# Kernel tuning notes

Hardware: AMD Instinct MI355X
Metric: run time of the kernel (lower is better)

Reference implementation:

```python
import jax, jax.numpy as jnp
import numpy as np

B, S, HID = 2, 2048, 2048
NH, NKV, D = 16, 8, 128
N_REP = NH // NKV
EPS = 1e-6
THETA = 10000.0


def setup_inputs() -> dict:
    key = jax.random.key(0)
    ks = jax.random.split(key, 6)
    s = 0.02
    return {
        "hidden_states": jax.random.normal(ks[0], (B, S, HID), jnp.float32),
        "attention_mask": jnp.ones((B, S), jnp.float32),
        "wq": jax.random.normal(ks[1], (HID, NH * D), jnp.float32) * s,
        "wk": jax.random.normal(ks[2], (HID, NKV * D), jnp.float32) * s,
        "wv": jax.random.normal(ks[3], (HID, NKV * D), jnp.float32) * s,
        "wo": jax.random.normal(ks[4], (NH * D, HID), jnp.float32) * s,
        "q_norm_w": jnp.ones((D,), jnp.float32),
        "k_norm_w": jnp.ones((D,), jnp.float32),
    }


def _rms_norm(x, w, eps=EPS):
    # x: (..., D); computed in fp32 like the torch module
    x32 = x.astype(jnp.float32)
    var = jnp.mean(x32 * x32, axis=-1, keepdims=True)
    return (w * (x32 * jax.lax.rsqrt(var + eps))).astype(x.dtype)


def _rotate_half(x):
    x1, x2 = jnp.split(x, 2, axis=-1)
    return jnp.concatenate((-x2, x1), axis=-1)


def _rope_cos_sin(seq_len, dim, dtype):
    inv_freq = 1.0 / (THETA ** (jnp.arange(0, dim, 2, dtype=jnp.float32) / dim))
    t = jnp.arange(seq_len, dtype=jnp.float32)
    freqs = t[:, None] * inv_freq[None, :]          # (S, D/2)
    emb = jnp.concatenate((freqs, freqs), axis=-1)  # (S, D)
    # broadcast to (1, 1, S, D)
    return jnp.cos(emb).astype(dtype)[None, None], jnp.sin(emb).astype(dtype)[None, None]


def reference(hidden_states, attention_mask, wq, wk, wv, wo, q_norm_w, k_norm_w):
    b, s, _ = hidden_states.shape
    # QKV projections (bias-free)
    q = (hidden_states @ wq).reshape(b, s, NH, D).transpose(0, 2, 1, 3)   # (b, nh, s, d)
    k = (hidden_states @ wk).reshape(b, s, NKV, D).transpose(0, 2, 1, 3)  # (b, nkv, s, d)
    v = (hidden_states @ wv).reshape(b, s, NKV, D).transpose(0, 2, 1, 3)
    # per-head QK RMSNorm
    q = _rms_norm(q, q_norm_w)
    k = _rms_norm(k, k_norm_w)
    # RoPE
    cos, sin = _rope_cos_sin(s, D, q.dtype)
    q = q * cos + _rotate_half(q) * sin
    k = k * cos + _rotate_half(k) * sin
    # GQA repeat kv heads
    k = jnp.repeat(k, N_REP, axis=1)
    v = jnp.repeat(v, N_REP, axis=1)
    # SDPA (bidirectional, additive padding mask)
    scale = 1.0 / np.sqrt(D)
    scores = jnp.einsum("bhqd,bhkd->bhqk", q, k) * scale
    add_mask = (1.0 - attention_mask)[:, None, None, :] * jnp.finfo(scores.dtype).min
    scores = scores + add_mask
    attn = jax.nn.softmax(scores, axis=-1)
    out = jnp.einsum("bhqk,bhkd->bhqd", attn, v)
    out = out.transpose(0, 2, 1, 3).reshape(b, s, NH * D)
    return out @ wo
```

## Files before the change

### kernel.cpp

```cpp
#include <hip/hip_runtime.h>
#include <stdint.h>

#define BB   2
#define SS   2048
#define HID  2048
#define NHQ  16
#define NKV  8
#define DD   128
#define QKVW 4096

typedef __bf16 v8bf   __attribute__((ext_vector_type(8)));
typedef float  f32x4  __attribute__((ext_vector_type(4)));
typedef float  f32x16 __attribute__((ext_vector_type(16)));

__device__ __forceinline__ float bf2f(ushort u) {
    union { unsigned int i; float f; } x; x.i = ((unsigned int)u) << 16; return x.f;
}
__device__ __forceinline__ ushort f2bf(float f) {
    union { float f; unsigned int i; } x; x.f = f;
    unsigned int i = x.i;
    return (ushort)((i + 0x7fffu + ((i >> 16) & 1u)) >> 16);
}
__device__ __forceinline__ v8bf as_bf8(uint4 u) { return __builtin_bit_cast(v8bf, u); }

__device__ __forceinline__ unsigned int cvtpk_bf16(float lo, float hi) {
    unsigned int r;
    asm("v_cvt_pk_bf16_f32 %0, %1, %2" : "=v"(r) : "v"(lo), "v"(hi));
    return r;
}

__device__ __forceinline__ void store_el(float* p, float v)  { *p = v; }
__device__ __forceinline__ void store_el(ushort* p, float v) { *p = f2bf(v); }

__device__ __forceinline__ void gll16(const ushort* g, ushort* l) {
    __builtin_amdgcn_global_load_lds(
        (const __attribute__((address_space(1))) void*)g,
        (__attribute__((address_space(3))) void*)l, 16, 0, 0);
}

#define PREP_CAST   8192
#define PREP_WQ     (PREP_CAST)
#define PREP_WK     (PREP_WQ + 4096)
#define PREP_WV     (PREP_WK + 2048)
#define PREP_WO     (PREP_WV + 2048)
#define PREP_TOTAL  (PREP_WO + 4096)

__device__ __forceinline__ void tcast_body(
    const float* __restrict__ in, ushort* __restrict__ out,
    int K, int N, int bx, int by, int t)
{
    __shared__ float tile[32][33];
    int n0 = bx * 32, k0 = by * 32;
    int tx = t & 31, ty = t >> 5;
#pragma unroll
    for (int i = 0; i < 32; i += 8)
        tile[ty + i][tx] = in[(size_t)(k0 + ty + i) * N + n0 + tx];
    __syncthreads();
#pragma unroll
    for (int i = 0; i < 32; i += 8)
        out[(size_t)(n0 + ty + i) * K + k0 + tx] = f2bf(tile[tx][ty + i]);
}

__global__ __launch_bounds__(256) void prep(
    const float* __restrict__ X,  const float* __restrict__ wq,
    const float* __restrict__ wk, const float* __restrict__ wv,
    const float* __restrict__ wo,
    ushort* __restrict__ Xb, ushort* __restrict__ WqkvT, ushort* __restrict__ Wot)
{
    int bid = blockIdx.x, t = threadIdx.x;
    if (bid < PREP_CAST) {
        int i = (bid * 256 + t) * 4;
        float4 v = *(const float4*)&X[i];
        ushort4 o = { f2bf(v.x), f2bf(v.y), f2bf(v.z), f2bf(v.w) };
        *(ushort4*)&Xb[i] = o;
    } else if (bid < PREP_WK) {
        int l = bid - PREP_WQ;
        tcast_body(wq, WqkvT, 2048, 2048, l & 63, l >> 6, t);
    } else if (bid < PREP_WV) {
        int l = bid - PREP_WK;
        tcast_body(wk, WqkvT + (size_t)2048 * 2048, 2048, 1024, l & 31, l >> 5, t);
    } else if (bid < PREP_WO) {
        int l = bid - PREP_WV;
        tcast_body(wv, WqkvT + (size_t)3072 * 2048, 2048, 1024, l & 31, l >> 5, t);
    } else {
        int l = bid - PREP_WO;
        tcast_body(wo, Wot, 2048, 2048, l & 63, l >> 6, t);
    }
}

template <typename OutT>
__global__ __launch_bounds__(256) void gemm_bt(
    const ushort* __restrict__ A, const ushort* __restrict__ Bt,
    OutT* __restrict__ C, int M, int N, int K)
{
    __shared__ __align__(16) ushort As[128 * 32];
    __shared__ __align__(16) ushort Bs[128 * 32];
    const int t = threadIdx.x;
    const int lane = t & 63, wave = t >> 6;
    const int quad = lane >> 4, l15 = lane & 15;
    const int m0 = blockIdx.y * 128, n0 = blockIdx.x * 128;
    const int wm = (wave >> 1) * 64, wn = (wave & 1) * 64;

    const f32x4 zv = {0.f, 0.f, 0.f, 0.f};
    f32x4 acc[4][4];
#pragma unroll
    for (int i = 0; i < 4; i++)
#pragma unroll
        for (int j = 0; j < 4; j++) acc[i][j] = zv;

    const int srow = t >> 2, sc8 = (t & 3) << 3;

    for (int k0 = 0; k0 < K; k0 += 32) {
        __syncthreads();
#pragma unroll
        for (int i = 0; i < 2; i++) {
            gll16(&A[(size_t)(m0 + srow + i * 64) * K + k0 + sc8], &As[(i * 256 + t) * 8]);
            gll16(&Bt[(size_t)(n0 + srow + i * 64) * K + k0 + sc8], &Bs[(i * 256 + t) * 8]);
        }
        __syncthreads();
        uint4 af[4], bf[4];
#pragma unroll
        for (int i = 0; i < 4; i++)
            af[i] = *(const uint4*)&As[(wm + i * 16 + l15) * 32 + quad * 8];
#pragma unroll
        for (int i = 0; i < 4; i++)
            bf[i] = *(const uint4*)&Bs[(wn + i * 16 + l15) * 32 + quad * 8];
#pragma unroll
        for (int mi = 0; mi < 4; mi++)
#pragma unroll
            for (int ni = 0; ni < 4; ni++)
                acc[mi][ni] = __builtin_amdgcn_mfma_f32_16x16x32_bf16(
                    as_bf8(af[mi]), as_bf8(bf[ni]), acc[mi][ni], 0, 0, 0);
    }
#pragma unroll
    for (int mi = 0; mi < 4; mi++)
#pragma unroll
        for (int ni = 0; ni < 4; ni++)
#pragma unroll
            for (int r = 0; r < 4; r++) {
                int row = m0 + wm + mi * 16 + quad * 4 + r;
                int col = n0 + wn + ni * 16 + l15;
                store_el(&C[(size_t)row * N + col], acc[mi][ni][r]);
            }
}

__global__ __launch_bounds__(256) void norm_rope(
    ushort* __restrict__ qkv, const float* __restrict__ qw, const float* __restrict__ kw)
{
    int row = blockIdx.x;
    int s = row & (SS - 1);
    int lane = threadIdx.x & 63, wave = threadIdx.x >> 6;
    int l = lane & 31, hsel = lane >> 5;
    float d0 = (float)(2 * l), d1 = d0 + 1.0f;
    float inv0 = expf(-d0 * (1.0f / 64.0f) * 9.210340371976184f);
    float inv1 = expf(-d1 * (1.0f / 64.0f) * 9.210340371976184f);
    float c0, s0, c1, s1;
    sincosf((float)s * inv0, &s0, &c0);
    sincosf((float)s * inv1, &s1, &c1);
    float qw0 = qw[2 * l], qw1 = qw[2 * l + 1], qy0 = qw[2 * l + 64], qy1 = qw[2 * l + 65];
    float kw0 = kw[2 * l], kw1 = kw[2 * l + 1], ky0 = kw[2 * l + 64], ky1 = kw[2 * l + 65];

#pragma unroll
    for (int pass = 0; pass < 3; pass++) {
        int h = pass * 8 + wave * 2 + hsel;
        ushort* p = qkv + (size_t)row * QKVW + h * 128;
        unsigned int ulo = *(const unsigned int*)&p[2 * l];
        unsigned int uhi = *(const unsigned int*)&p[2 * l + 64];
        float x0 = bf2f((ushort)ulo), x1 = bf2f((ushort)(ulo >> 16));
        float y0 = bf2f((ushort)uhi), y1 = bf2f((ushort)(uhi >> 16));
        float ssum = x0 * x0 + x1 * x1 + y0 * y0 + y1 * y1;
#pragma unroll
        for (int xm = 1; xm < 32; xm <<= 1) ssum += __shfl_xor(ssum, xm, 64);
        float r = rsqrtf(ssum * (1.0f / 128.0f) + 1e-6f);
        bool isq = (h < 16);
        float w0 = isq ? qw0 : kw0, w1 = isq ? qw1 : kw1;
        float v0 = isq ? qy0 : ky0, v1 = isq ? qy1 : ky1;
        float sc = isq ? 0.08838834764831845f : 1.0f;
        float nx0 = w0 * (x0 * r), nx1 = w1 * (x1 * r);
        float ny0 = v0 * (y0 * r), ny1 = v1 * (y1 * r);
        float ox0 = (nx0 * c0 - ny0 * s0) * sc, ox1 = (nx1 * c1 - ny1 * s1) * sc;
        float oy0 = (ny0 * c0 + nx0 * s0) * sc, oy1 = (ny1 * c1 + nx1 * s1) * sc;
        *(unsigned int*)&p[2 * l]      = (unsigned int)f2bf(ox0) | ((unsigned int)f2bf(ox1) << 16);
        *(unsigned int*)&p[2 * l + 64] = (unsigned int)f2bf(oy0) | ((unsigned int)f2bf(oy1) << 16);
    }
}

__global__ __launch_bounds__(256, 2) void flash_attn(
    const ushort* __restrict__ qkv, const float* __restrict__ mask, ushort* __restrict__ O)
{
    __shared__ __align__(16) ushort Ks[64 * 128];
    __shared__ __align__(16) ushort Vt[128 * 64];
    __shared__ __align__(16) float  Madd[SS];
    const int t = threadIdx.x;
    const int lane = t & 63, wave = t >> 6;
    const int l31 = lane & 31, half = lane >> 5;
    const int b = blockIdx.z, h = blockIdx.y, q0 = blockIdx.x * 128;
    const int kh = h >> 1;

#pragma unroll
    for (int i = 0; i < 2; i++) {
        int idx = i * 1024 + t * 4;
        float4 mv = *(const float4*)&mask[b * SS + idx];
        float4 o = { (1.f - mv.x) * -1e30f, (1.f - mv.y) * -1e30f,
                     (1.f - mv.z) * -1e30f, (1.f - mv.w) * -1e30f };
        *(float4*)&Madd[idx] = o;
    }

    uint4 aq[8];
    {
        const ushort* qp = qkv + ((size_t)(b * SS + q0 + wave * 32 + l31)) * QKVW + h * 128 + half * 8;
#pragma unroll
        for (int kt = 0; kt < 8; kt++) aq[kt] = *(const uint4*)&qp[kt * 16];
    }
    f32x16 acc_o[4];
#pragma unroll
    for (int i = 0; i < 4; i++)
#pragma unroll
        for (int r = 0; r < 16; r++) acc_o[i][r] = 0.f;
    float lp[4] = {0.f, 0.f, 0.f, 0.f};

    const ushort* Kg = qkv + (size_t)b * SS * QKVW + 2048 + kh * 128;
    const ushort* Vg = qkv + (size_t)b * SS * QKVW + 3072 + kh * 128;

    const int vp = t & 31, vdc = t >> 5;
    uint4 vreg[4];
#define LOAD_V(K0)                                                                  \
    {                                                                               \
        _Pragma("unroll")                                                           \
        for (int pass = 0; pass < 2; pass++) {                                      \
            int d0 = (vdc + pass * 8) * 8;                                          \
            vreg[pass * 2 + 0] = *(const uint4*)&Vg[(size_t)((K0) + 2 * vp) * QKVW + d0];     \
            vreg[pass * 2 + 1] = *(const uint4*)&Vg[(size_t)((K0) + 2 * vp + 1) * QKVW + d0]; \
        }                                                                           \
    }
    LOAD_V(0);

    for (int k0 = 0; k0 < SS; k0 += 64) {
        __syncthreads();
#pragma unroll
        for (int i = 0; i < 4; i++) {
            int chunk = i * 256 + t;
            int row = chunk >> 4, cp = chunk & 15;
            int cl = cp ^ (row & 15);
            gll16(&Kg[(size_t)(k0 + row) * QKVW + cl * 8], &Ks[chunk * 8]);
        }
#pragma unroll
        for (int pass = 0; pass < 2; pass++) {
            const ushort* pa_ = (const ushort*)&vreg[pass * 2 + 0];
            const ushort* pb_ = (const ushort*)&vreg[pass * 2 + 1];
            int d0 = (vdc + pass * 8) * 8;
#pragma unroll
            for (int j = 0; j < 8; j++) {
                int cp = (vp >> 2) ^ j;
                unsigned int v = (unsigned int)pa_[j] | ((unsigned int)pb_[j] << 16);
                *(unsigned int*)&Vt[(d0 + j) * 64 + cp * 8 + (vp & 3) * 2] = v;
            }
        }
        __syncthreads();
        if (k0 + 64 < SS) LOAD_V(k0 + 64);

        f32x16 sc[2];
        __builtin_amdgcn_s_setprio(1);
#pragma unroll
        for (int nt = 0; nt < 2; nt++) {
#pragma unroll
            for (int r = 0; r < 16; r++) sc[nt][r] = 0.f;
#pragma unroll
            for (int kt = 0; kt < 8; kt++) {
                int cp = (kt * 2 + half) ^ (l31 & 15);
                uint4 bk = *(const uint4*)&Ks[(nt * 32 + l31) * 128 + cp * 8];
                sc[nt] = __builtin_amdgcn_mfma_f32_32x32x16_bf16(
                    as_bf8(bk), as_bf8(aq[kt]), sc[nt], 0, 0, 0);
            }
        }
        __builtin_amdgcn_s_setprio(0);

        uint4 pa[4];
#pragma unroll
        for (int nt = 0; nt < 2; nt++) {
            float p[16];
#pragma unroll
            for (int g = 0; g < 4; g++) {
                f32x4 em = *(const f32x4*)&Madd[k0 + nt * 32 + 4 * half + g * 8];
#pragma unroll
                for (int j = 0; j < 4; j++) {
                    int r = g * 4 + j;
                    float pv = __expf(sc[nt][r] + em[j]);
                    p[r] = pv;
                    lp[j] += pv;
                }
            }
            unsigned int pk[8];
#pragma unroll
            for (int i = 0; i < 8; i++) pk[i] = cvtpk_bf16(p[2 * i], p[2 * i + 1]);
            auto sA = __builtin_amdgcn_permlane32_swap(pk[0], pk[2], false, false);
            auto sB = __builtin_amdgcn_permlane32_swap(pk[1], pk[3], false, false);
            auto sC = __builtin_amdgcn_permlane32_swap(pk[4], pk[6], false, false);
            auto sD = __builtin_amdgcn_permlane32_swap(pk[5], pk[7], false, false);
            uint4 f0, f1;
            f0.x = sA[0]; f0.y = sB[0]; f0.z = sA[1]; f0.w = sB[1];
            f1.x = sC[0]; f1.y = sD[0]; f1.z = sC[1]; f1.w = sD[1];
            pa[nt * 2 + 0] = f0;
            pa[nt * 2 + 1] = f1;
        }

        __builtin_amdgcn_s_setprio(1);
#pragma unroll
        for (int kt2 = 0; kt2 < 4; kt2++) {
            int kc = kt2 * 2 + half;
            int co = (kc ^ (l31 & 7)) * 8;
#pragma unroll
            for (int nt = 0; nt < 4; nt++) {
                uint4 bv = *(const uint4*)&Vt[(nt * 32 + l31) * 64 + co];
                acc_o[nt] = __builtin_amdgcn_mfma_f32_32x32x16_bf16(
                    as_bf8(pa[kt2]), as_bf8(bv), acc_o[nt], 0, 0, 0);
            }
        }
        __builtin_amdgcn_s_setprio(0);
    }
    float lsum = (lp[0] + lp[1]) + (lp[2] + lp[3]);
    lsum += __shfl_xor(lsum, 32, 64);
    float linv = 1.0f / lsum;
    float li[16];
#pragma unroll
    for (int r = 0; r < 16; r++)
        li[r] = __shfl(linv, (r & 3) + 8 * (r >> 2) + 4 * half, 64);
#pragma unroll
    for (int nt = 0; nt < 4; nt++)
#pragma unroll
        for (int r = 0; r < 16; r++) {
            int prow = (r & 3) + 8 * (r >> 2) + 4 * half;
            int qrow = q0 + wave * 32 + prow;
            int d = nt * 32 + l31;
            float v = acc_o[nt][r] * li[r];
            O[((size_t)(b * SS + qrow)) * (NHQ * DD) + h * 128 + d] = f2bf(v);
        }
}

extern "C" void kernel_launch(void* const* d_in, const int* in_sizes, int n_in,
                              void* d_out, int out_size, void* d_ws, size_t ws_size,
                              hipStream_t stream)
{
    const float* X    = (const float*)d_in[0];
    const float* mask = (const float*)d_in[1];
    const float* wq   = (const float*)d_in[2];
    const float* wk   = (const float*)d_in[3];
    const float* wv   = (const float*)d_in[4];
    const float* wo   = (const float*)d_in[5];
    const float* qnw  = (const float*)d_in[6];
    const float* knw  = (const float*)d_in[7];
    float* out = (float*)d_out;

    const size_t M = (size_t)BB * SS;
    ushort* Xb    = (ushort*)d_ws;
    ushort* WqkvT = Xb    + M * HID;
    ushort* Wot   = WqkvT + (size_t)4096 * HID;
    ushort* QKV   = Wot   + (size_t)2048 * 2048;
    ushort* Obuf  = QKV   + M * QKVW;

    prep<<<PREP_TOTAL, 256, 0, stream>>>(X, wq, wk, wv, wo, Xb, WqkvT, Wot);

    gemm_bt<ushort><<<dim3(4096 / 128, 4096 / 128), 256, 0, stream>>>(Xb, WqkvT, QKV, 4096, 4096, 2048);

    norm_rope<<<(int)M, 256, 0, stream>>>(QKV, qnw, knw);

    flash_attn<<<dim3(SS / 128, NHQ, BB), 256, 0, stream>>>(QKV, mask, Obuf);

    gemm_bt<float><<<dim3(2048 / 128, 4096 / 128), 256, 0, stream>>>(Obuf, Wot, out, 4096, 2048, 2048);
}
```

Measured before the change: 394.3 us.

## Rewrite GEMM with triple-buffered LDS pipeline, swizzled layout, and 256x128 tiles

Replaces the single-buffered 128x128 GEMM with a 512-thread, 256x128-tile kernel. It uses a 3-stage global_load_lds pipeline over K=64 chunks, an XOR-swizzled LDS layout to avoid bank conflicts, and split MFMA phases with setprio and explicit waitcnt and barriers. The aim is to hide global-load latency and raise reuse per tile. Costs are a large LDS footprint (~144KB per block) that limits occupancy, and fragile hand-tuned synchronization.

```diff
diff --git a/kernel.cpp b/kernel.cpp
--- a/kernel.cpp
+++ b/kernel.cpp
@@ -36,6 +36,10 @@
     __builtin_amdgcn_global_load_lds(
         (const __attribute__((address_space(1))) void*)g,
         (__attribute__((address_space(3))) void*)l, 16, 0, 0);
+}
+
+__device__ __forceinline__ int swz_off(int r, int lcolb) {
+    return r * 64 + (((lcolb) ^ ((r & 4) << 3)) >> 1);
 }
 
 #define PREP_CAST   8192
@@ -89,17 +93,18 @@
 }
 
 template <typename OutT>
-__global__ __launch_bounds__(256) void gemm_bt(
+__global__ __launch_bounds__(512, 2) void gemm_bt2(
     const ushort* __restrict__ A, const ushort* __restrict__ Bt,
     OutT* __restrict__ C, int M, int N, int K)
 {
-    __shared__ __align__(16) ushort As[128 * 32];
-    __shared__ __align__(16) ushort Bs[128 * 32];
+    __shared__ __align__(16) ushort As[3][256 * 64];
+    __shared__ __align__(16) ushort Bs[3][128 * 64];
     const int t = threadIdx.x;
     const int lane = t & 63, wave = t >> 6;
     const int quad = lane >> 4, l15 = lane & 15;
-    const int m0 = blockIdx.y * 128, n0 = blockIdx.x * 128;
-    const int wm = (wave >> 1) * 64, wn = (wave & 1) * 64;
+    const int m0 = blockIdx.y * 256, n0 = blockIdx.x * 128;
+    const int wm = (wave >> 1) * 64;
+    const int wn = (wave & 1) * 64;
 
     const f32x4 zv = {0.f, 0.f, 0.f, 0.f};
     f32x4 acc[4][4];
@@ -108,39 +113,130 @@
 #pragma unroll
         for (int j = 0; j < 4; j++) acc[i][j] = zv;
 
-    const int srow = t >> 2, sc8 = (t & 3) << 3;
-
-    for (int k0 = 0; k0 < K; k0 += 32) {
-        __syncthreads();
-#pragma unroll
-        for (int i = 0; i < 2; i++) {
-            gll16(&A[(size_t)(m0 + srow + i * 64) * K + k0 + sc8], &As[(i * 256 + t) * 8]);
-            gll16(&Bt[(size_t)(n0 + srow + i * 64) * K + k0 + sc8], &Bs[(i * 256 + t) * 8]);
-        }
-        __syncthreads();
-        uint4 af[4], bf[4];
-#pragma unroll
-        for (int i = 0; i < 4; i++)
-            af[i] = *(const uint4*)&As[(wm + i * 16 + l15) * 32 + quad * 8];
-#pragma unroll
-        for (int i = 0; i < 4; i++)
-            bf[i] = *(const uint4*)&Bs[(wn + i * 16 + l15) * 32 + quad * 8];
-#pragma unroll
-        for (int mi = 0; mi < 4; mi++)
-#pragma unroll
-            for (int ni = 0; ni < 4; ni++)
-                acc[mi][ni] = __builtin_amdgcn_mfma_f32_16x16x32_bf16(
-                    as_bf8(af[mi]), as_bf8(bf[ni]), acc[mi][ni], 0, 0, 0);
-    }
-#pragma unroll
-    for (int mi = 0; mi < 4; mi++)
-#pragma unroll
-        for (int ni = 0; ni < 4; ni++)
+    int arow[4], acol[4];
+#pragma unroll
+    for (int j = 0; j < 4; j++) {
+        int p = (j * 512 + t) * 16;
+        int l = p ^ (((p >> 9) & 1) << 5);
+        arow[j] = l >> 7; acol[j] = (l & 127) >> 1;
+    }
+    int brow[2], bcol[2];
+#pragma unroll
+    for (int j = 0; j < 2; j++) {
+        int p = (j * 512 + t) * 16;
+        int l = p ^ (((p >> 9) & 1) << 5);
+        brow[j] = l >> 7; bcol[j] = (l & 127) >> 1;
+    }
+
+    int aoff[4][2], boff[2][2][2];
+#pragma unroll
+    for (int mf = 0; mf < 4; mf++)
+#pragma unroll
+        for (int kk = 0; kk < 2; kk++)
+            aoff[mf][kk] = swz_off(wm + mf * 16 + l15, kk * 64 + quad * 16);
+#pragma unroll
+    for (int q = 0; q < 2; q++)
+#pragma unroll
+        for (int nf = 0; nf < 2; nf++)
+#pragma unroll
+            for (int kk = 0; kk < 2; kk++)
+                boff[q][nf][kk] = swz_off(wn + q * 32 + nf * 16 + l15, kk * 64 + quad * 16);
+
+#define STAGE_A(j, slot, kk0) \
+    gll16(&A[(size_t)(m0 + arow[j]) * K + (kk0) + acol[j]], &As[slot][0] + ((j) * 512 + t) * 8)
+#define STAGE_B(j, slot, kk0) \
+    gll16(&Bt[(size_t)(n0 + brow[j]) * K + (kk0) + bcol[j]], &Bs[slot][0] + ((j) * 512 + t) * 8)
+
+    const int NT = K >> 6;
+
+#pragma unroll
+    for (int j = 0; j < 4; j++) STAGE_A(j, 0, 0);
+#pragma unroll
+    for (int j = 0; j < 2; j++) STAGE_B(j, 0, 0);
+#pragma unroll
+    for (int j = 0; j < 4; j++) STAGE_A(j, 1, 64);
+#pragma unroll
+    for (int j = 0; j < 2; j++) STAGE_B(j, 1, 64);
+    asm volatile("s_waitcnt vmcnt(6)" ::: "memory");
+    __builtin_amdgcn_s_barrier();
+
+    int cur = 0;
+    for (int T = 0; T < NT; T++) {
+        const ushort* Ac = &As[cur][0];
+        const ushort* Bc = &Bs[cur][0];
+        int stg = cur + 2; if (stg >= 3) stg -= 3;
+        const int k2 = (T + 2) << 6;
+        const bool do_stage = (T + 2) < NT;
+
+        uint4 af[4][2], bf[2][2];
+#pragma unroll
+        for (int mf = 0; mf < 4; mf++)
+#pragma unroll
+            for (int kk = 0; kk < 2; kk++)
+                af[mf][kk] = *(const uint4*)&Ac[aoff[mf][kk]];
+#pragma unroll
+        for (int nf = 0; nf < 2; nf++)
+#pragma unroll
+            for (int kk = 0; kk < 2; kk++)
+                bf[nf][kk] = *(const uint4*)&Bc[boff[0][nf][kk]];
+        if (do_stage) {
+            STAGE_A(0, stg, k2); STAGE_A(1, stg, k2); STAGE_B(0, stg, k2);
+        }
+        __builtin_amdgcn_s_barrier();
+        asm volatile("s_waitcnt lgkmcnt(0)" ::: "memory");
+        __builtin_amdgcn_sched_barrier(0);
+        __builtin_amdgcn_s_setprio(1);
+#pragma unroll
+        for (int mf = 0; mf < 4; mf++)
+#pragma unroll
+            for (int nf = 0; nf < 2; nf++)
+#pragma unroll
+                for (int kk = 0; kk < 2; kk++)
+                    acc[mf][nf] = __builtin_amdgcn_mfma_f32_16x16x32_bf16(
+                        as_bf8(af[mf][kk]), as_bf8(bf[nf][kk]), acc[mf][nf], 0, 0, 0);
+        __builtin_amdgcn_s_setprio(0);
+        __builtin_amdgcn_s_barrier();
+
+#pragma unroll
+        for (int nf = 0; nf < 2; nf++)
+#pragma unroll
+            for (int kk = 0; kk < 2; kk++)
+                bf[nf][kk] = *(const uint4*)&Bc[boff[1][nf][kk]];
+        if (do_stage) {
+            STAGE_A(2, stg, k2); STAGE_A(3, stg, k2); STAGE_B(1, stg, k2);
+            asm volatile("s_waitcnt vmcnt(6)" ::: "memory");
+        } else if (T + 2 == NT) {
+            asm volatile("s_waitcnt vmcnt(0)" ::: "memory");
+        }
+        __builtin_amdgcn_s_barrier();
+        asm volatile("s_waitcnt lgkmcnt(0)" ::: "memory");
+        __builtin_amdgcn_sched_barrier(0);
+        __builtin_amdgcn_s_setprio(1);
+#pragma unroll
+        for (int mf = 0; mf < 4; mf++)
+#pragma unroll
+            for (int nf = 0; nf < 2; nf++)
+#pragma unroll
+                for (int kk = 0; kk < 2; kk++)
+                    acc[mf][2 + nf] = __builtin_amdgcn_mfma_f32_16x16x32_bf16(
+                        as_bf8(af[mf][kk]), as_bf8(bf[nf][kk]), acc[mf][2 + nf], 0, 0, 0);
+        __builtin_amdgcn_s_setprio(0);
+        __builtin_amdgcn_s_barrier();
+
+        cur++; if (cur == 3) cur = 0;
+    }
+#undef STAGE_A
+#undef STAGE_B
+
+#pragma unroll
+    for (int mf = 0; mf < 4; mf++)
+#pragma unroll
+        for (int nf = 0; nf < 4; nf++)
 #pragma unroll
             for (int r = 0; r < 4; r++) {
-                int row = m0 + wm + mi * 16 + quad * 4 + r;
-                int col = n0 + wn + ni * 16 + l15;
-                store_el(&C[(size_t)row * N + col], acc[mi][ni][r]);
+                int row = m0 + wm + mf * 16 + quad * 4 + r;
+                int col = n0 + wn + nf * 16 + l15;
+                store_el(&C[(size_t)row * N + col], acc[mf][nf][r]);
             }
 }
 
@@ -360,11 +456,11 @@
 
     prep<<<PREP_TOTAL, 256, 0, stream>>>(X, wq, wk, wv, wo, Xb, WqkvT, Wot);
 
-    gemm_bt<ushort><<<dim3(4096 / 128, 4096 / 128), 256, 0, stream>>>(Xb, WqkvT, QKV, 4096, 4096, 2048);
+    gemm_bt2<ushort><<<dim3(4096 / 128, 4096 / 256), 512, 0, stream>>>(Xb, WqkvT, QKV, 4096, 4096, 2048);
 
     norm_rope<<<(int)M, 256, 0, stream>>>(QKV, qnw, knw);
 
     flash_attn<<<dim3(SS / 128, NHQ, BB), 256, 0, stream>>>(QKV, mask, Obuf);
 
-    gemm_bt<float><<<dim3(2048 / 128, 4096 / 128), 256, 0, stream>>>(Obuf, Wot, out, 4096, 2048, 2048);
-}
+    gemm_bt2<float><<<dim3(2048 / 128, 4096 / 256), 512, 0, stream>>>(Obuf, Wot, out, 4096, 2048, 2048);
+}
```

New measurement: 352.3 us. 10.7% less time.
